# Kernel tuning notes

Hardware: AMD Instinct MI355X
Metric: run time of the kernel (lower is better)

Reference implementation:

```python
import jax, jax.numpy as jnp
import numpy as np

B, C, H, W = 8, 1024, 64, 64

def setup_inputs() -> dict:
    key = jax.random.key(0)
    k1, k2, k3, k4 = jax.random.split(key, 4)
    return {
        "prev_key": jax.random.normal(k1, (B, C, H, W), dtype=jnp.float32),
        "prev_value": jax.random.normal(k2, (B, C, H, W), dtype=jnp.float32),
        "curr_key": jax.random.normal(k3, (B, C, H, W), dtype=jnp.float32),
        "curr_value": jax.random.normal(k4, (B, C, H, W), dtype=jnp.float32),
    }


def _get_affinity(mk, qk):
    # mk, qk: [B, CK, N]  (N = H*W)
    CK = mk.shape[1]
    a_sq = jnp.sum(mk * mk, axis=1)[:, :, None]          # [B, N, 1]
    ab = jnp.einsum('bcn,bcm->bnm', mk, qk)              # [B, N, N]
    affinity = (2.0 * ab - a_sq) / jnp.sqrt(jnp.asarray(CK, mk.dtype))
    # softmax over memory positions (dim 1), numerically stable
    return jax.nn.softmax(affinity, axis=1)              # [B, N, N]


def reference(prev_key, prev_value, curr_key, curr_value):
    b, ck, h, w = prev_key.shape
    n = h * w
    mk = prev_key.reshape(b, ck, n)
    qk = curr_key.reshape(b, ck, n)
    affinity = _get_affinity(mk, qk)                     # [B, N, N]
    cv = prev_value.shape[1]
    mo = prev_value.reshape(b, cv, n)                    # [B, CV, N]
    mem = jnp.einsum('bcn,bnm->bcm', mo, affinity)       # [B, CV, N]
    mem = mem.reshape(b, cv, h, w)
    return jnp.concatenate([mem, curr_value], axis=1)    # [B, 2*CV, H, W]
```

## Files before the change

### kernel.cpp

```cpp
#include <hip/hip_runtime.h>
#include <hip/hip_bf16.h>

#define BATCH 8
#define CH    1024
#define NN    4096

typedef __attribute__((ext_vector_type(8))) short bf16x8;
typedef __attribute__((ext_vector_type(4))) float f32x4;
using bf16 = __hip_bfloat16;

struct bhalf4 { bf16 x, y, z, w; };

__device__ __forceinline__ unsigned short f2bfu(float f) {
  bf16 h = __float2bfloat16(f);
  return *reinterpret_cast<unsigned short*>(&h);
}

template <bool ASQ>
__global__ __launch_bounds__(256) void transpose_cast_v(
    const float* __restrict__ in_all, bf16* __restrict__ out_all,
    float* __restrict__ asq_all) {
  int bz = blockIdx.z;
  const float* in = in_all + (size_t)bz * CH * NN;
  bf16* out = out_all + (size_t)bz * NN * CH;

  __shared__ float tile[64][65];
  __shared__ float sqb[16][64];

  int n0 = blockIdx.x * 64;
  int c0 = blockIdx.y * 64;
  int t = threadIdx.x;
  int nc = t & 15;
  int cr = t >> 4;

  float4 sq4 = make_float4(0.f, 0.f, 0.f, 0.f);
#pragma unroll
  for (int i = 0; i < 4; ++i) {
    int c = cr + i * 16;
    float4 v = *(const float4*)(in + (size_t)(c0 + c) * NN + n0 + nc * 4);
    tile[c][nc * 4 + 0] = v.x;
    tile[c][nc * 4 + 1] = v.y;
    tile[c][nc * 4 + 2] = v.z;
    tile[c][nc * 4 + 3] = v.w;
    if (ASQ) {
      sq4.x += v.x * v.x; sq4.y += v.y * v.y;
      sq4.z += v.z * v.z; sq4.w += v.w * v.w;
    }
  }
  if (ASQ) {
    sqb[cr][nc * 4 + 0] = sq4.x;
    sqb[cr][nc * 4 + 1] = sq4.y;
    sqb[cr][nc * 4 + 2] = sq4.z;
    sqb[cr][nc * 4 + 3] = sq4.w;
  }
  __syncthreads();
  if (ASQ && t < 64) {
    float s = 0.f;
#pragma unroll
    for (int i = 0; i < 16; ++i) s += sqb[i][t];
    atomicAdd(&asq_all[(size_t)bz * NN + n0 + t], s);
  }
  int cchunk = t & 7;
  int nb = t >> 3;
#pragma unroll
  for (int p = 0; p < 2; ++p) {
    int n = nb + p * 32;
    bf16x8 o;
#pragma unroll
    for (int j = 0; j < 8; ++j)
      o[j] = (short)f2bfu(tile[cchunk * 8 + j][n]);
    *(bf16x8*)(out + (size_t)(n0 + n) * CH + c0 + cchunk * 8) = o;
  }
}

__global__ __launch_bounds__(256) void convert_cast(
    const float4* __restrict__ in, bhalf4* __restrict__ out) {
  size_t i = (size_t)blockIdx.x * 256 + threadIdx.x;
  float4 v = in[i];
  bhalf4 o;
  o.x = __float2bfloat16(v.x);
  o.y = __float2bfloat16(v.y);
  o.z = __float2bfloat16(v.z);
  o.w = __float2bfloat16(v.w);
  out[i] = o;
}

#define BARR() __builtin_amdgcn_s_barrier()
#define PRIO(x) __builtin_amdgcn_s_setprio(x)
#define LDS_FENCE() do {                                      \
    asm volatile("s_waitcnt lgkmcnt(0)" ::: "memory");        \
    __builtin_amdgcn_sched_barrier(0);                        \
  } while (0)
#define MEM_FENCE() do {                                      \
    asm volatile("" ::: "memory");                            \
    __builtin_amdgcn_sched_barrier(0);                        \
  } while (0)

__device__ __forceinline__ void gload16(const bf16* g, bf16* l) {
  __builtin_amdgcn_global_load_lds(
      (const __attribute__((address_space(1))) void*)g,
      (__attribute__((address_space(3))) void*)l, 16, 0, 0);
}

template <int K, int MODE, int TM, int TN>
__global__ __launch_bounds__(256, 3) void gemm_s3(
    const bf16* __restrict__ Aall, const bf16* __restrict__ Ball,
    bf16* __restrict__ Pall, float* __restrict__ Oall,
    const float* __restrict__ asq_all, float* __restrict__ rsum_all) {
  constexpr int NT = K / 32;
  constexpr int TPB = TM * TN;
  constexpr int NWG = TPB * BATCH;
  constexpr int GRP = 8;

  int lid = blockIdx.x;
  int swz = (lid & 7) * (NWG >> 3) + (lid >> 3);
  int bz  = swz / TPB;
  int rem = swz - bz * TPB;
  int g  = rem / (GRP * TN);
  int r2 = rem - g * (GRP * TN);
  int bx = r2 / GRP;
  int by = g * GRP + (r2 & (GRP - 1));

  const bf16* Ab = Aall + (size_t)bz * TM * 128 * K + (size_t)(by * 128) * K;
  const bf16* Bb = Ball + (size_t)bz * TN * 128 * K + (size_t)(bx * 128) * K;

  __shared__ bf16 As[3][128 * 32];
  __shared__ bf16 Bs[3][128 * 32];
  bf16* const AsB = &As[0][0];
  bf16* const BsB = &Bs[0][0];

  int tid = threadIdx.x;
  int wv = tid >> 6, lane = tid & 63;
  int fl = lane & 15, quad = lane >> 4;
  int wr = wv >> 1, wc = wv & 1;

  int r0 = tid >> 2;
  int c0 = (tid & 3) ^ ((r0 >> 1) & 3);
  int r1 = (256 + tid) >> 2;
  int c1 = ((256 + tid) & 3) ^ ((r1 >> 1) & 3);
  const bf16* gA0 = Ab + (size_t)r0 * K + c0 * 8;
  const bf16* gA1 = Ab + (size_t)r1 * K + c1 * 8;
  const bf16* gB0 = Bb + (size_t)r0 * K + c0 * 8;
  const bf16* gB1 = Bb + (size_t)r1 * K + c1 * 8;
  int ls0 = wv * 512;
  int ls1 = 2048 + wv * 512;

  int kq = (quad ^ ((fl >> 1) & 3)) * 8;
  int aoff = (wr * 64 + fl) * 32 + kq;
  int boff = (wc * 64 + fl) * 32 + kq;

  f32x4 acc[4][4] = {};

#define STAGE2() do {                                                         \
    bf16* da = AsB + sb * 4096;                                               \
    bf16* db = BsB + sb * 4096;                                               \
    gload16(gA0, da + ls0); gload16(gA1, da + ls1);                           \
    gload16(gB0, db + ls0); gload16(gB1, db + ls1);                           \
    gA0 += 32; gA1 += 32; gB0 += 32; gB1 += 32;                               \
  } while (0)

  {
    int sb = 0; STAGE2();
    sb = 1; STAGE2();
  }
  asm volatile("s_waitcnt vmcnt(4)" ::: "memory");
  BARR();

  int cb = 0, sb = 2;
  for (int t = 0; t < NT; ++t) {
    const bf16* Ac = AsB + cb * 4096;
    const bf16* Bc = BsB + cb * 4096;
    bf16x8 aF[4], bF[4];
#pragma unroll
    for (int mi = 0; mi < 4; ++mi)
      aF[mi] = *(const bf16x8*)(Ac + aoff + mi * 512);
#pragma unroll
    for (int nj = 0; nj < 4; ++nj)
      bF[nj] = *(const bf16x8*)(Bc + boff + nj * 512);

    if (t + 2 < NT) STAGE2();

    BARR();
    asm volatile("s_waitcnt lgkmcnt(0)" ::: "memory");
    __builtin_amdgcn_sched_barrier(0);
    PRIO(1);
#pragma unroll
    for (int mi = 0; mi < 4; ++mi)
#pragma unroll
      for (int nj = 0; nj < 4; ++nj)
        acc[mi][nj] = __builtin_amdgcn_mfma_f32_16x16x32_bf16(
            aF[mi], bF[nj], acc[mi][nj], 0, 0, 0);
    PRIO(0);
    if (t + 2 < NT) {
      asm volatile("s_waitcnt vmcnt(4)" ::: "memory");
    } else {
      asm volatile("s_waitcnt vmcnt(0)" ::: "memory");
    }
    BARR();

    cb = (cb == 2) ? 0 : cb + 1;
    sb = (sb == 2) ? 0 : sb + 1;
  }
#undef STAGE2

  __syncthreads();

  int colbase = bx * 128 + wc * 64;
  int rowg0 = by * 128 + wr * 64;

  if constexpr (MODE == 0) {
    const float* asq = asq_all + (size_t)bz * NN;
    float* rsum = rsum_all + (size_t)bz * NN;
    bf16* P = Pall + (size_t)bz * NN * NN;
    short* scr = (short*)AsB + wv * 1024;

    float aq[4];
#pragma unroll
    for (int nj = 0; nj < 4; ++nj) aq[nj] = asq[colbase + nj * 16 + fl];

    float rs[4][4];
#pragma unroll
    for (int mi = 0; mi < 4; ++mi)
#pragma unroll
      for (int r = 0; r < 4; ++r) rs[mi][r] = 0.f;

#pragma unroll
    for (int mi = 0; mi < 4; ++mi) {
#pragma unroll
      for (int nj = 0; nj < 4; ++nj)
#pragma unroll
        for (int r = 0; r < 4; ++r) {
          int row = (quad << 2) + r;
          float e = __expf((2.f * acc[mi][nj][r] - aq[nj]) * 0.03125f);
          rs[mi][r] += e;
          int chunk = (nj * 2 + (fl >> 3)) ^ (row & 7);
          scr[row * 64 + chunk * 8 + (fl & 7)] = (short)f2bfu(e);
        }
      LDS_FENCE();
#pragma unroll
      for (int p = 0; p < 2; ++p) {
        int row = (p << 3) + (lane >> 3);
        int c = lane & 7;
        int chunk = c ^ (row & 7);
        bf16x8 v = *(const bf16x8*)(scr + row * 64 + chunk * 8);
        *(bf16x8*)(P + (size_t)(rowg0 + mi * 16 + row) * NN + colbase + c * 8) = v;
      }
      MEM_FENCE();
    }
#pragma unroll
    for (int mi = 0; mi < 4; ++mi)
#pragma unroll
      for (int r = 0; r < 4; ++r) {
        float v = rs[mi][r];
        v += __shfl_xor(v, 1);
        v += __shfl_xor(v, 2);
        v += __shfl_xor(v, 4);
        v += __shfl_xor(v, 8);
        if (fl == 0)
          atomicAdd(&rsum[rowg0 + mi * 16 + (quad << 2) + r], v);
      }
  } else {
    float* Co = Oall + (size_t)bz * 2 * CH * NN;
    const float* rsum = rsum_all + (size_t)bz * NN;
    float* scr = (float*)AsB + wv * 1024;

    float inv[4];
#pragma unroll
    for (int nj = 0; nj < 4; ++nj) inv[nj] = 1.f / rsum[colbase + nj * 16 + fl];

#pragma unroll
    for (int mi = 0; mi < 4; ++mi) {
#pragma unroll
      for (int nj = 0; nj < 4; ++nj)
#pragma unroll
        for (int r = 0; r < 4; ++r) {
          int row = (quad << 2) + r;
          int chunk = (nj * 4 + (fl >> 2)) ^ (row & 15);
          scr[row * 64 + chunk * 4 + (fl & 3)] = acc[mi][nj][r] * inv[nj];
        }
      LDS_FENCE();
#pragma unroll
      for (int p = 0; p < 4; ++p) {
        int row = (p << 2) + (lane >> 4);
        int c = lane & 15;
        int chunk = c ^ (row & 15);
        f32x4 v = *(const f32x4*)(scr + row * 64 + chunk * 4);
        *(f32x4*)(Co + (size_t)(rowg0 + mi * 16 + row) * NN + colbase + c * 4) = v;
      }
      MEM_FENCE();
    }
  }
}

__global__ __launch_bounds__(256) void copy_curr(
    const float4* __restrict__ src, float4* __restrict__ dst) {
  size_t idx = (size_t)blockIdx.x * 256 + threadIdx.x;
  size_t b = idx >> 20;
  size_t r = idx & 1048575;
  dst[b * 2097152 + 1048576 + r] = src[idx];
}

extern "C" void kernel_launch(void* const* d_in, const int* in_sizes, int n_in,
                              void* d_out, int out_size, void* d_ws, size_t ws_size,
                              hipStream_t stream) {
  const float* prev_key   = (const float*)d_in[0];
  const float* prev_value = (const float*)d_in[1];
  const float* curr_key   = (const float*)d_in[2];
  const float* curr_value = (const float*)d_in[3];
  float* out = (float*)d_out;

  char* ws = (char*)d_ws;
  bf16* P     = (bf16*)(ws);
  bf16* mk_t  = (bf16*)(ws + 268435456u);
  bf16* qk_t  = (bf16*)(ws + 335544320u);
  bf16* mo_b  = (bf16*)(ws + 402653184u);
  float* a_sq = (float*)(ws + 469762048u);
  float* rsum = a_sq + (size_t)BATCH * NN;

  hipMemsetAsync(a_sq, 0, 2ull * BATCH * NN * sizeof(float), stream);

  transpose_cast_v<true><<<dim3(NN / 64, CH / 64, BATCH), 256, 0, stream>>>(
      prev_key, mk_t, a_sq);
  transpose_cast_v<false><<<dim3(NN / 64, CH / 64, BATCH), 256, 0, stream>>>(
      curr_key, qk_t, nullptr);
  convert_cast<<<(size_t)BATCH * CH * NN / 4 / 256, 256, 0, stream>>>(
      (const float4*)prev_value, (bhalf4*)mo_b);

  gemm_s3<CH, 0, 32, 32><<<dim3(32 * 32 * BATCH), dim3(256), 0, stream>>>(
      qk_t, mk_t, P, nullptr, a_sq, rsum);

  gemm_s3<NN, 1, 8, 32><<<dim3(8 * 32 * BATCH), dim3(256), 0, stream>>>(
      mo_b, P, nullptr, out, nullptr, rsum);

  copy_curr<<<(size_t)BATCH * CH * NN / 4 / 256, 256, 0, stream>>>(
      (const float4*)curr_value, (float4*)out);
}
```

Baseline: 1.266 ms.

## Double-buffer LDS fragment registers and unroll GEMM main loop by two

Restructures the GEMM K-loop so LDS fragment reads for the next tile are issued before the MFMAs on the current tile, using two register fragment sets and a loop unrolled by two. The aim is to hide LDS read latency behind matrix-core work instead of waiting on it each iteration. The cost is more VGPRs, which could lower occupancy, plus more complex barrier and waitcnt ordering across the three-stage LDS ring. It assumes an even tile count.

```diff
diff --git a/kernel.cpp b/kernel.cpp
--- a/kernel.cpp
+++ b/kernel.cpp
@@ -150,58 +150,78 @@
   int boff = (wc * 64 + fl) * 32 + kq;
 
   f32x4 acc[4][4] = {};
-
-#define STAGE2() do {                                                         \
-    bf16* da = AsB + sb * 4096;                                               \
-    bf16* db = BsB + sb * 4096;                                               \
+  bf16x8 a0[4], b0[4], a1[4], b1[4];
+
+#define STAGE2(SB) do {                                                       \
+    bf16* da = AsB + (SB) * 4096;                                             \
+    bf16* db = BsB + (SB) * 4096;                                             \
     gload16(gA0, da + ls0); gload16(gA1, da + ls1);                           \
     gload16(gB0, db + ls0); gload16(gB1, db + ls1);                           \
     gA0 += 32; gA1 += 32; gB0 += 32; gB1 += 32;                               \
   } while (0)
 
-  {
-    int sb = 0; STAGE2();
-    sb = 1; STAGE2();
-  }
+#define RDFRAGS(AF, BF, CB) do {                                              \
+    const bf16* Ac_ = AsB + (CB) * 4096;                                      \
+    const bf16* Bc_ = BsB + (CB) * 4096;                                      \
+    _Pragma("unroll")                                                         \
+    for (int mi_ = 0; mi_ < 4; ++mi_)                                         \
+      AF[mi_] = *(const bf16x8*)(Ac_ + aoff + mi_ * 512);                     \
+    _Pragma("unroll")                                                         \
+    for (int nj_ = 0; nj_ < 4; ++nj_)                                         \
+      BF[nj_] = *(const bf16x8*)(Bc_ + boff + nj_ * 512);                     \
+  } while (0)
+
+#define DOMFMA(AF, BF) do {                                                   \
+    PRIO(1);                                                                  \
+    _Pragma("unroll")                                                         \
+    for (int mi_ = 0; mi_ < 4; ++mi_)                                         \
+      _Pragma("unroll")                                                       \
+      for (int nj_ = 0; nj_ < 4; ++nj_)                                       \
+        acc[mi_][nj_] = __builtin_amdgcn_mfma_f32_16x16x32_bf16(              \
+            AF[mi_], BF[nj_], acc[mi_][nj_], 0, 0, 0);                        \
+    PRIO(0);                                                                  \
+  } while (0)
+
+  STAGE2(0);
+  STAGE2(1);
   asm volatile("s_waitcnt vmcnt(4)" ::: "memory");
   BARR();
-
-  int cb = 0, sb = 2;
-  for (int t = 0; t < NT; ++t) {
-    const bf16* Ac = AsB + cb * 4096;
-    const bf16* Bc = BsB + cb * 4096;
-    bf16x8 aF[4], bF[4];
-#pragma unroll
-    for (int mi = 0; mi < 4; ++mi)
-      aF[mi] = *(const bf16x8*)(Ac + aoff + mi * 512);
-#pragma unroll
-    for (int nj = 0; nj < 4; ++nj)
-      bF[nj] = *(const bf16x8*)(Bc + boff + nj * 512);
-
-    if (t + 2 < NT) STAGE2();
+  RDFRAGS(a0, b0, 0);
+
+  int cb = 0;
+  for (int t = 0; t < NT; t += 2) {
+    int nb = cb + 1; if (nb == 3) nb = 0;
+    int s2 = nb + 1; if (s2 == 3) s2 = 0;
 
     BARR();
     asm volatile("s_waitcnt lgkmcnt(0)" ::: "memory");
     __builtin_amdgcn_sched_barrier(0);
-    PRIO(1);
-#pragma unroll
-    for (int mi = 0; mi < 4; ++mi)
-#pragma unroll
-      for (int nj = 0; nj < 4; ++nj)
-        acc[mi][nj] = __builtin_amdgcn_mfma_f32_16x16x32_bf16(
-            aF[mi], bF[nj], acc[mi][nj], 0, 0, 0);
-    PRIO(0);
     if (t + 2 < NT) {
+      STAGE2(s2);
       asm volatile("s_waitcnt vmcnt(4)" ::: "memory");
     } else {
       asm volatile("s_waitcnt vmcnt(0)" ::: "memory");
     }
+    RDFRAGS(a1, b1, nb);
+    DOMFMA(a0, b0);
+
     BARR();
-
-    cb = (cb == 2) ? 0 : cb + 1;
-    sb = (sb == 2) ? 0 : sb + 1;
+    asm volatile("s_waitcnt lgkmcnt(0)" ::: "memory");
+    __builtin_amdgcn_sched_barrier(0);
+    if (t + 3 < NT) {
+      STAGE2(cb);
+      asm volatile("s_waitcnt vmcnt(4)" ::: "memory");
+    } else {
+      asm volatile("s_waitcnt vmcnt(0)" ::: "memory");
+    }
+    if (t + 2 < NT) RDFRAGS(a0, b0, s2);
+    DOMFMA(a1, b1);
+
+    cb = s2;
   }
 #undef STAGE2
+#undef RDFRAGS
+#undef DOMFMA
 
   __syncthreads();
 
```

New measurement: 1.318 ms. 1.04x slower.

## Enlarge GEMM block tile to 256x128 with 8x4 MFMA fragments per wave

Applied to the files above, without the earlier changes.

Doubles the M dimension of each workgroup tile in both GEMMs from 128 to 256 rows, so each wave computes 128x64 outputs with 32 accumulators. The LDS A buffers are enlarged, the loads per stage rise to six, and the waitcnt thresholds are adjusted to match. The grid sizes are halved, occupancy is lowered to 2 workgroups per CU, and the swizzle group size is capped for the smaller TM. The goal is more MFMA work per LDS fragment load and less global and LDS traffic per FLOP, at the cost of higher register pressure and fewer resident waves.

```diff
diff --git a/kernel.cpp b/kernel.cpp
--- a/kernel.cpp
+++ b/kernel.cpp
@@ -103,14 +103,14 @@
 }
 
 template <int K, int MODE, int TM, int TN>
-__global__ __launch_bounds__(256, 3) void gemm_s3(
+__global__ __launch_bounds__(256, 2) void gemm_s3(
     const bf16* __restrict__ Aall, const bf16* __restrict__ Ball,
     bf16* __restrict__ Pall, float* __restrict__ Oall,
     const float* __restrict__ asq_all, float* __restrict__ rsum_all) {
   constexpr int NT = K / 32;
   constexpr int TPB = TM * TN;
   constexpr int NWG = TPB * BATCH;
-  constexpr int GRP = 8;
+  constexpr int GRP = (TM < 8) ? TM : 8;
 
   int lid = blockIdx.x;
   int swz = (lid & 7) * (NWG >> 3) + (lid >> 3);
@@ -121,10 +121,10 @@
   int bx = r2 / GRP;
   int by = g * GRP + (r2 & (GRP - 1));
 
-  const bf16* Ab = Aall + (size_t)bz * TM * 128 * K + (size_t)(by * 128) * K;
+  const bf16* Ab = Aall + (size_t)bz * TM * 256 * K + (size_t)(by * 256) * K;
   const bf16* Bb = Ball + (size_t)bz * TN * 128 * K + (size_t)(bx * 128) * K;
 
-  __shared__ bf16 As[3][128 * 32];
+  __shared__ bf16 As[3][256 * 32];
   __shared__ bf16 Bs[3][128 * 32];
   bf16* const AsB = &As[0][0];
   bf16* const BsB = &Bs[0][0];
@@ -134,65 +134,65 @@
   int fl = lane & 15, quad = lane >> 4;
   int wr = wv >> 1, wc = wv & 1;
 
-  int r0 = tid >> 2;
-  int c0 = (tid & 3) ^ ((r0 >> 1) & 3);
-  int r1 = (256 + tid) >> 2;
-  int c1 = ((256 + tid) & 3) ^ ((r1 >> 1) & 3);
-  const bf16* gA0 = Ab + (size_t)r0 * K + c0 * 8;
-  const bf16* gA1 = Ab + (size_t)r1 * K + c1 * 8;
-  const bf16* gB0 = Bb + (size_t)r0 * K + c0 * 8;
-  const bf16* gB1 = Bb + (size_t)r1 * K + c1 * 8;
-  int ls0 = wv * 512;
-  int ls1 = 2048 + wv * 512;
+  int rA0 = tid >> 2,           cA0 = (tid & 3) ^ ((rA0 >> 1) & 3);
+  int rA1 = (256 + tid) >> 2,   cA1 = ((256 + tid) & 3) ^ ((rA1 >> 1) & 3);
+  int rA2 = (512 + tid) >> 2,   cA2 = ((512 + tid) & 3) ^ ((rA2 >> 1) & 3);
+  int rA3 = (768 + tid) >> 2,   cA3 = ((768 + tid) & 3) ^ ((rA3 >> 1) & 3);
+  const bf16* gA0 = Ab + (size_t)rA0 * K + cA0 * 8;
+  const bf16* gA1 = Ab + (size_t)rA1 * K + cA1 * 8;
+  const bf16* gA2 = Ab + (size_t)rA2 * K + cA2 * 8;
+  const bf16* gA3 = Ab + (size_t)rA3 * K + cA3 * 8;
+  const bf16* gB0 = Bb + (size_t)rA0 * K + cA0 * 8;
+  const bf16* gB1 = Bb + (size_t)rA1 * K + cA1 * 8;
+  int lsu = wv * 512;
 
   int kq = (quad ^ ((fl >> 1) & 3)) * 8;
-  int aoff = (wr * 64 + fl) * 32 + kq;
+  int aoff = (wr * 128 + fl) * 32 + kq;
   int boff = (wc * 64 + fl) * 32 + kq;
 
-  f32x4 acc[4][4] = {};
-
-#define STAGE2() do {                                                         \
-    bf16* da = AsB + sb * 4096;                                               \
-    bf16* db = BsB + sb * 4096;                                               \
-    gload16(gA0, da + ls0); gload16(gA1, da + ls1);                           \
-    gload16(gB0, db + ls0); gload16(gB1, db + ls1);                           \
-    gA0 += 32; gA1 += 32; gB0 += 32; gB1 += 32;                               \
+  f32x4 acc[8][4] = {};
+
+#define STAGE2(SB) do {                                                       \
+    bf16* da = AsB + (SB) * 8192;                                             \
+    bf16* db = BsB + (SB) * 4096;                                             \
+    gload16(gA0, da + lsu);        gload16(gA1, da + 2048 + lsu);             \
+    gload16(gA2, da + 4096 + lsu); gload16(gA3, da + 6144 + lsu);             \
+    gload16(gB0, db + lsu);        gload16(gB1, db + 2048 + lsu);             \
+    gA0 += 32; gA1 += 32; gA2 += 32; gA3 += 32; gB0 += 32; gB1 += 32;         \
   } while (0)
 
-  {
-    int sb = 0; STAGE2();
-    sb = 1; STAGE2();
-  }
-  asm volatile("s_waitcnt vmcnt(4)" ::: "memory");
+  STAGE2(0);
+  STAGE2(1);
+  asm volatile("s_waitcnt vmcnt(6)" ::: "memory");
   BARR();
 
   int cb = 0, sb = 2;
   for (int t = 0; t < NT; ++t) {
-    const bf16* Ac = AsB + cb * 4096;
+    const bf16* Ac = AsB + cb * 8192;
     const bf16* Bc = BsB + cb * 4096;
-    bf16x8 aF[4], bF[4];
-#pragma unroll
-    for (int mi = 0; mi < 4; ++mi)
+    bf16x8 aF[8], bF[4];
+#pragma unroll
+    for (int mi = 0; mi < 8; ++mi)
       aF[mi] = *(const bf16x8*)(Ac + aoff + mi * 512);
 #pragma unroll
     for (int nj = 0; nj < 4; ++nj)
       bF[nj] = *(const bf16x8*)(Bc + boff + nj * 512);
 
-    if (t + 2 < NT) STAGE2();
+    if (t + 2 < NT) STAGE2(sb);
 
     BARR();
     asm volatile("s_waitcnt lgkmcnt(0)" ::: "memory");
     __builtin_amdgcn_sched_barrier(0);
     PRIO(1);
 #pragma unroll
-    for (int mi = 0; mi < 4; ++mi)
+    for (int mi = 0; mi < 8; ++mi)
 #pragma unroll
       for (int nj = 0; nj < 4; ++nj)
         acc[mi][nj] = __builtin_amdgcn_mfma_f32_16x16x32_bf16(
             aF[mi], bF[nj], acc[mi][nj], 0, 0, 0);
     PRIO(0);
     if (t + 2 < NT) {
-      asm volatile("s_waitcnt vmcnt(4)" ::: "memory");
+      asm volatile("s_waitcnt vmcnt(6)" ::: "memory");
     } else {
       asm volatile("s_waitcnt vmcnt(0)" ::: "memory");
     }
@@ -206,7 +206,7 @@
   __syncthreads();
 
   int colbase = bx * 128 + wc * 64;
-  int rowg0 = by * 128 + wr * 64;
+  int rowg0 = by * 256 + wr * 128;
 
   if constexpr (MODE == 0) {
     const float* asq = asq_all + (size_t)bz * NN;
@@ -218,14 +218,14 @@
 #pragma unroll
     for (int nj = 0; nj < 4; ++nj) aq[nj] = asq[colbase + nj * 16 + fl];
 
-    float rs[4][4];
-#pragma unroll
-    for (int mi = 0; mi < 4; ++mi)
+    float rs[8][4];
+#pragma unroll
+    for (int mi = 0; mi < 8; ++mi)
 #pragma unroll
       for (int r = 0; r < 4; ++r) rs[mi][r] = 0.f;
 
 #pragma unroll
-    for (int mi = 0; mi < 4; ++mi) {
+    for (int mi = 0; mi < 8; ++mi) {
 #pragma unroll
       for (int nj = 0; nj < 4; ++nj)
 #pragma unroll
@@ -248,7 +248,7 @@
       MEM_FENCE();
     }
 #pragma unroll
-    for (int mi = 0; mi < 4; ++mi)
+    for (int mi = 0; mi < 8; ++mi)
 #pragma unroll
       for (int r = 0; r < 4; ++r) {
         float v = rs[mi][r];
@@ -269,7 +269,7 @@
     for (int nj = 0; nj < 4; ++nj) inv[nj] = 1.f / rsum[colbase + nj * 16 + fl];
 
 #pragma unroll
-    for (int mi = 0; mi < 4; ++mi) {
+    for (int mi = 0; mi < 8; ++mi) {
 #pragma unroll
       for (int nj = 0; nj < 4; ++nj)
 #pragma unroll
@@ -326,10 +326,10 @@
   convert_cast<<<(size_t)BATCH * CH * NN / 4 / 256, 256, 0, stream>>>(
       (const float4*)prev_value, (bhalf4*)mo_b);
 
-  gemm_s3<CH, 0, 32, 32><<<dim3(32 * 32 * BATCH), dim3(256), 0, stream>>>(
+  gemm_s3<CH, 0, 16, 32><<<dim3(16 * 32 * BATCH), dim3(256), 0, stream>>>(
       qk_t, mk_t, P, nullptr, a_sq, rsum);
 
-  gemm_s3<NN, 1, 8, 32><<<dim3(8 * 32 * BATCH), dim3(256), 0, stream>>>(
+  gemm_s3<NN, 1, 4, 32><<<dim3(4 * 32 * BATCH), dim3(256), 0, stream>>>(
       mo_b, P, nullptr, out, nullptr, rsum);
 
   copy_curr<<<(size_t)BATCH * CH * NN / 4 / 256, 256, 0, stream>>>(
```

After: 1.187 ms. 6.3% less time.
